# Kernel tuning notes

Measured on AMD Instinct MI355X. Metric: run time of the kernel, lower is better.

Reference implementation:

```python
import jax, jax.numpy as jnp
import numpy as np

EPS_BN = 1e-5
EPS_NORM = 1e-12

def _proj(x, W, g, b, m, v):
    # x: (B,C,N); W: (O,C) 1x1 conv; eval-mode BN per out channel; ReLU
    y = jnp.einsum('oc,bcn->bon', W, x)
    s = g / jnp.sqrt(v + EPS_BN)
    y = (y - m[None, :, None]) * s[None, :, None] + b[None, :, None]
    return jax.nn.relu(y)

def _l2norm(x, axis):
    n = jnp.sqrt(jnp.sum(x * x, axis=axis, keepdims=True))
    return x / jnp.maximum(n, EPS_NORM)

def setup_inputs() -> dict:
    key = jax.random.key(0)
    ks = jax.random.split(key, 8)
    B, C, H, W = 8, 256, 96, 96
    NS, K = 256, 64  # num_state, K
    X = jax.random.normal(ks[0], (B, C, H, W), dtype=jnp.float32)
    def mk(k, out_c):
        return (jax.random.normal(k, (out_c, C), dtype=jnp.float32) * 0.05,
                jnp.ones((out_c,), jnp.float32), jnp.zeros((out_c,), jnp.float32),
                jnp.zeros((out_c,), jnp.float32), jnp.ones((out_c,), jnp.float32))
    phi_w, phi_g, phi_b, phi_m, phi_v = mk(ks[1], K)
    theta_w, theta_g, theta_b, theta_m, theta_v = mk(ks[2], NS)
    rou_w, rou_g, rou_b, rou_m, rou_v = mk(ks[3], NS)
    val_w, val_g, val_b, val_m, val_v = mk(ks[4], NS)
    return dict(X=X,
                phi_w=phi_w, phi_g=phi_g, phi_b=phi_b, phi_m=phi_m, phi_v=phi_v,
                theta_w=theta_w, theta_g=theta_g, theta_b=theta_b, theta_m=theta_m, theta_v=theta_v,
                rou_w=rou_w, rou_g=rou_g, rou_b=rou_b, rou_m=rou_m, rou_v=rou_v,
                val_w=val_w, val_g=val_g, val_b=val_b, val_m=val_m, val_v=val_v)

def reference(X, phi_w, phi_g, phi_b, phi_m, phi_v,
              theta_w, theta_g, theta_b, theta_m, theta_v,
              rou_w, rou_g, rou_b, rou_m, rou_v,
              val_w, val_g, val_b, val_m, val_v):
    B, C, H, W = X.shape
    N = H * W
    x = X.reshape(B, C, N)
    x_phi = _proj(x, phi_w, phi_g, phi_b, phi_m, phi_v)          # (B,K,N)
    x_theta = _proj(x, theta_w, theta_g, theta_b, theta_m, theta_v)  # (B,S,N)
    x_theta = jax.nn.softmax(x_theta, axis=-1)                   # softmax over N
    discrib = jnp.einsum('bkn,bsn->bks', x_phi, x_theta)         # (B,K,S)
    x_rou = _proj(x, rou_w, rou_g, rou_b, rou_m, rou_v)          # (B,S,N)
    x_rou = jax.nn.softmax(x_rou, axis=1)                        # softmax over channels S
    Q = jnp.einsum('bks,bsn->bnk', discrib, x_rou)               # (B,N,K)
    Q = _l2norm(Q, axis=1)                                       # F.normalize dim=1 (over N)
    Q = jax.nn.softmax(Q, axis=-1)                               # softmax over K
    x_val = _proj(x, val_w, val_g, val_b, val_m, val_v)          # (B,S,N)
    # Z = sum_n Q[b,n,k]*x_val[b,s,n] / sum_n Q[b,n,k]  -- batched GEMM, no (B,S,N,K) blowup
    Znum = jnp.einsum('bsn,bnk->bsk', x_val, Q)                  # (B,S,K)
    Z = Znum / Q.sum(axis=1)[:, None, :]
    Z = _l2norm(Z, axis=1)                                       # F.normalize dim=1 (over S)
    return (Z, Q)
```

## Files before the change

### kernel.cpp

```cpp
#include <hip/hip_runtime.h>
#include <math.h>

#define B_ 8
#define C_ 256
#define N_ 9216
#define S_ 256
#define K_ 64
#define NCHUNK 36
#define TILE_KS (K_ * S_)
#define NC8 (N_ / 8)

typedef unsigned short ushort_t;
typedef __attribute__((ext_vector_type(8))) short bf16x8;
typedef __attribute__((ext_vector_type(4))) float f32x4;

static __device__ inline ushort_t f2bf(float x) {
    unsigned int u = __float_as_uint(x);
    unsigned int r = (u + 0x7fffu + ((u >> 16) & 1u)) >> 16;
    return (ushort_t)r;
}
static __device__ inline float bf2f(ushort_t u) {
    return __uint_as_float(((unsigned int)u) << 16);
}
static __device__ inline unsigned int cvtpk(float lo, float hi) {
    unsigned int r;
    asm("v_cvt_pk_bf16_f32 %0, %1, %2" : "=v"(r) : "v"(lo), "v"(hi));
    return r;
}

static __device__ inline uint4 expcell(uint4 u, float2 s) {
    uint4 r;
    unsigned int* up = (unsigned int*)&u;
    unsigned int* rp = (unsigned int*)&r;
#pragma unroll
    for (int q = 0; q < 4; ++q) {
        unsigned int x = up[q];
        float lo = __uint_as_float((x & 0xffffu) << 16);
        float hi = __uint_as_float(x & 0xffff0000u);
        rp[q] = cvtpk(__expf(lo - s.x) * s.y, __expf(hi - s.x) * s.y);
    }
    return r;
}

__global__ __launch_bounds__(256) void prep_w(
    const float* __restrict__ phi_w, const float* __restrict__ phi_g, const float* __restrict__ phi_b,
    const float* __restrict__ phi_m, const float* __restrict__ phi_v,
    const float* __restrict__ th_w, const float* __restrict__ th_g, const float* __restrict__ th_b,
    const float* __restrict__ th_m, const float* __restrict__ th_v,
    const float* __restrict__ ro_w, const float* __restrict__ ro_g, const float* __restrict__ ro_b,
    const float* __restrict__ ro_m, const float* __restrict__ ro_v,
    const float* __restrict__ va_w, const float* __restrict__ va_g, const float* __restrict__ va_b,
    const float* __restrict__ va_m, const float* __restrict__ va_v,
    ushort_t* __restrict__ Wt, float* __restrict__ be)
{
    const int o = blockIdx.x;
    const int t = threadIdx.x;
    const float *src, *g, *bb, *mm, *vv; int orel;
    if (o < 64)       { src = phi_w; g = phi_g; bb = phi_b; mm = phi_m; vv = phi_v; orel = o; }
    else if (o < 320) { src = th_w;  g = th_g;  bb = th_b;  mm = th_m;  vv = th_v;  orel = o - 64; }
    else if (o < 576) { src = ro_w;  g = ro_g;  bb = ro_b;  mm = ro_m;  vv = ro_v;  orel = o - 320; }
    else              { src = va_w;  g = va_g;  bb = va_b;  mm = va_m;  vv = va_v;  orel = o - 576; }
    const float s = g[orel] / sqrtf(vv[orel] + 1e-5f);
    const int ot = o >> 6, os = (o >> 4) & 3, st = t >> 5;
    const size_t flat = ((((size_t)ot * 8 + st) * 4 + os) * 64 + ((t >> 3) & 3) * 16 + (o & 15)) * 8 + (t & 7);
    Wt[flat] = f2bf(src[orel * C_ + t] * s);
    if (t == 0) be[o] = bb[orel] - mm[orel] * s;
}

__global__ __launch_bounds__(256) void xpose(
    const float* __restrict__ X, ushort_t* __restrict__ Xs)
{
    __shared__ float T[64][65];
    const int b = blockIdx.z, c0 = blockIdx.y * 64, n0 = blockIdx.x * 64;
    const int t = threadIdx.x;
#pragma unroll
    for (int p = 0; p < 4; ++p) {
        int c = p * 16 + (t >> 4), nn = (t & 15) * 4;
        float4 v = *(const float4*)&X[((size_t)b * C_ + c0 + c) * N_ + n0 + nn];
        T[c][nn] = v.x; T[c][nn + 1] = v.y; T[c][nn + 2] = v.z; T[c][nn + 3] = v.w;
    }
    __syncthreads();
#pragma unroll
    for (int p = 0; p < 4; ++p) {
        int nn = p * 16 + (t >> 4), cl = (t & 15) * 4;
        uint2 uu;
        uu.x = cvtpk(T[cl][nn], T[cl + 1][nn]);
        uu.y = cvtpk(T[cl + 2][nn], T[cl + 3][nn]);
        const int n = n0 + nn, c = c0 + cl;
        const int nt = n >> 8, nr = n & 255;
        const int st = c >> 5, g8 = (c >> 3) & 3, e = c & 7;
        const size_t base = ((((size_t)b * 36 + nt) * 8 + st) * 1024
                             + (nr >> 4) * 64 + g8 * 16 + (nr & 15)) * 8 + e;
        *(uint2*)&Xs[base] = uu;
    }
}

__global__ __launch_bounds__(256) void proj_mfma_all(
    const ushort_t* __restrict__ Wt, const float* __restrict__ be,
    const ushort_t* __restrict__ Xs,
    ushort_t* __restrict__ Pbf, ushort_t* __restrict__ Tbf,
    ushort_t* __restrict__ Vbf, ushort_t* __restrict__ Rt)
{
    __shared__ short sm[9216];
    const int t = threadIdx.x;
    const int l = t & 63, w = t >> 6;
    const int idx = blockIdx.x;
    const int xcd = idx & 7, pos = idx >> 3;
    const int vid = xcd * 468 + pos;
    const int ot  = vid % 13;
    const int r   = vid / 13;
    const int b   = r / 36;
    const int nt  = r % 36;
    const int n0  = nt * 256;
    const int o0  = ot * 64;

    const bf16x8* Wv = (const bf16x8*)Wt;
    const bf16x8* Xf = (const bf16x8*)Xs;
    const size_t xbase = ((size_t)b * 36 + nt) * 8192;
    const size_t wbase = (size_t)ot * 2048;
    const int boff = (l >> 4) * 16 + (l & 15);

    f32x4 zr = {0.f, 0.f, 0.f, 0.f};
    f32x4 acc[4][4];
#pragma unroll
    for (int i = 0; i < 4; ++i)
#pragma unroll
        for (int j = 0; j < 4; ++j) acc[i][j] = zr;

    bf16x8 A0[4], B0[4];
#pragma unroll
    for (int os = 0; os < 4; ++os) A0[os] = Wv[wbase + os * 64 + l];
#pragma unroll
    for (int j = 0; j < 4; ++j)   B0[j]  = Xf[xbase + (w * 4 + j) * 64 + boff];

#pragma unroll
    for (int st = 0; st < 8; ++st) {
        bf16x8 A1[4], B1[4];
        if (st < 7) {
#pragma unroll
            for (int os = 0; os < 4; ++os)
                A1[os] = Wv[wbase + (st + 1) * 256 + os * 64 + l];
#pragma unroll
            for (int j = 0; j < 4; ++j)
                B1[j] = Xf[xbase + (size_t)(st + 1) * 1024 + (w * 4 + j) * 64 + boff];
        }
#pragma unroll
        for (int os = 0; os < 4; ++os)
#pragma unroll
            for (int j = 0; j < 4; ++j)
                acc[os][j] = __builtin_amdgcn_mfma_f32_16x16x32_bf16(A0[os], B0[j], acc[os][j], 0, 0, 0);
#pragma unroll
        for (int os = 0; os < 4; ++os) A0[os] = A1[os];
#pragma unroll
        for (int j = 0; j < 4; ++j)   B0[j]  = B1[j];
    }

    if (o0 >= 320 && o0 < 576) {
        const int od = o0 - 320;
        ushort_t* Tt = (ushort_t*)sm + w * (32 * 72);
#pragma unroll
        for (int half = 0; half < 2; ++half) {
            __syncthreads();
#pragma unroll
            for (int jj = 0; jj < 2; ++jj) {
                const int j = half * 2 + jj;
                const int row = jj * 16 + (l & 15);
#pragma unroll
                for (int os = 0; os < 4; ++os) {
                    const int scol0 = os * 16 + (l >> 4) * 4;
                    const float b0 = be[o0 + scol0], b1 = be[o0 + scol0 + 1];
                    const float b2 = be[o0 + scol0 + 2], b3 = be[o0 + scol0 + 3];
                    unsigned int p0 = cvtpk(fmaxf(acc[os][j][0] + b0, 0.f),
                                            fmaxf(acc[os][j][1] + b1, 0.f));
                    unsigned int p1 = cvtpk(fmaxf(acc[os][j][2] + b2, 0.f),
                                            fmaxf(acc[os][j][3] + b3, 0.f));
                    *(unsigned int*)&Tt[row * 72 + scol0]     = p0;
                    *(unsigned int*)&Tt[row * 72 + scol0 + 2] = p1;
                }
            }
            __syncthreads();
#pragma unroll
            for (int p = 0; p < 4; ++p) {
                const int lrow = p * 8 + (l >> 3);
                uint4 v = *(const uint4*)&Tt[lrow * 72 + (l & 7) * 8];
                *(uint4*)&Rt[((size_t)b * N_ + n0 + w * 64 + half * 32 + lrow) * 256 + od + (l & 7) * 8] = v;
            }
        }
    } else {
        ushort_t* dst; int od, osz;
        if (o0 < 64)       { dst = Pbf; od = o0;       osz = 64;  }
        else if (o0 < 320) { dst = Tbf; od = o0 - 64;  osz = 256; }
        else               { dst = Vbf; od = o0 - 576; osz = 256; }
        ushort_t* Tw = (ushort_t*)sm + w * (32 * 68);
        const int c = l & 15;
#pragma unroll
        for (int half = 0; half < 2; ++half) {
            __syncthreads();
#pragma unroll
            for (int osl = 0; osl < 2; ++osl) {
                const int os = half * 2 + osl;
#pragma unroll
                for (int r2 = 0; r2 < 4; ++r2) {
                    const int lrow = osl * 16 + (l >> 4) * 4 + r2;
                    const int orow = half * 32 + lrow;
                    const float bias = be[o0 + orow];
                    unsigned int p0 = cvtpk(fmaxf(acc[os][0][r2] + bias, 0.f),
                                            fmaxf(acc[os][1][r2] + bias, 0.f));
                    unsigned int p1 = cvtpk(fmaxf(acc[os][2][r2] + bias, 0.f),
                                            fmaxf(acc[os][3][r2] + bias, 0.f));
                    Tw[lrow * 68 + c]      = (ushort_t)p0;
                    Tw[lrow * 68 + 16 + c] = (ushort_t)(p0 >> 16);
                    Tw[lrow * 68 + 32 + c] = (ushort_t)p1;
                    Tw[lrow * 68 + 48 + c] = (ushort_t)(p1 >> 16);
                }
            }
            __syncthreads();
#pragma unroll
            for (int i = 0; i < 8; ++i) {
                const int lrow = i * 4 + (l >> 4);
                ushort4 v = *(const ushort4*)&Tw[lrow * 68 + (l & 15) * 4];
                *(ushort4*)&dst[((size_t)(b * osz + od + half * 32 + lrow)) * N_ + n0 + w * 64 + (l & 15) * 4] = v;
            }
        }
    }
}

__global__ __launch_bounds__(256) void rowstat_n(
    const ushort_t* __restrict__ T, float* __restrict__ st2)
{
    const int row = blockIdx.x;
    const ushort4* p = (const ushort4*)(T + (size_t)row * N_);
    const int t = threadIdx.x;
    float v[36];
    float mx = -INFINITY;
#pragma unroll
    for (int i = 0; i < 9; ++i) {
        ushort4 u = p[t + i * 256];
        v[i * 4 + 0] = bf2f(u.x); v[i * 4 + 1] = bf2f(u.y);
        v[i * 4 + 2] = bf2f(u.z); v[i * 4 + 3] = bf2f(u.w);
        mx = fmaxf(mx, fmaxf(fmaxf(v[i * 4], v[i * 4 + 1]), fmaxf(v[i * 4 + 2], v[i * 4 + 3])));
    }
    __shared__ float red[256];
    red[t] = mx; __syncthreads();
    for (int s2 = 128; s2 > 0; s2 >>= 1) {
        if (t < s2) red[t] = fmaxf(red[t], red[t + s2]);
        __syncthreads();
    }
    mx = red[0]; __syncthreads();
    float sum = 0.f;
#pragma unroll
    for (int i = 0; i < 36; ++i) sum += __expf(v[i] - mx);
    red[t] = sum; __syncthreads();
    for (int s2 = 128; s2 > 0; s2 >>= 1) {
        if (t < s2) red[t] += red[t + s2];
        __syncthreads();
    }
    if (t == 0) ((float2*)st2)[row] = make_float2(mx, 1.0f / red[0]);
}

__global__ __launch_bounds__(256) void rowstat_rt(
    const ushort_t* __restrict__ R, float* __restrict__ st2r)
{
    const int w = threadIdx.x >> 6, l = threadIdx.x & 63;
    const size_t row0 = (size_t)blockIdx.x * 32 + w * 8;
    for (int r = 0; r < 8; ++r) {
        const ushort4* p = (const ushort4*)(R + (row0 + r) * 256);
        ushort4 u = p[l];
        float f0 = bf2f(u.x), f1 = bf2f(u.y), f2 = bf2f(u.z), f3 = bf2f(u.w);
        float mx = fmaxf(fmaxf(f0, f1), fmaxf(f2, f3));
#pragma unroll
        for (int m = 1; m < 64; m <<= 1) mx = fmaxf(mx, __shfl_xor(mx, m));
        float s = __expf(f0 - mx) + __expf(f1 - mx) + __expf(f2 - mx) + __expf(f3 - mx);
#pragma unroll
        for (int m = 1; m < 64; m <<= 1) s += __shfl_xor(s, m);
        if (l == 0) ((float2*)st2r)[row0 + r] = make_float2(mx, 1.0f / s);
    }
}

__global__ __launch_bounds__(256) void ks_mfma(
    const ushort_t* __restrict__ A, const ushort_t* __restrict__ Bm,
    const float* __restrict__ st2, float* __restrict__ P)
{
    __shared__ short sm[32768];
    const int t = threadIdx.x;
    const int l = t & 63, w = t >> 6;
    const int chunk = blockIdx.x, b = blockIdx.y;
    const int ccell = chunk * 32;

    const uint4* Av = (const uint4*)A;
    const uint4* Bv = (const uint4*)Bm;
    const float2* S2 = (const float2*)st2;
    uint4* smv = (uint4*)sm;
    const bool doexp = (st2 != nullptr);

    uint4 wreg[8], xreg[8];
    float2 sreg[8];
#pragma unroll
    for (int i = 0; i < 8; ++i) {
        int cell = i * 256 + t;
        int osub = cell >> 9, g = (cell >> 4) & 31, oi = cell & 15;
        wreg[i] = Av[(size_t)(b * 64 + osub * 16 + oi) * NC8 + ccell + g];
    }
#pragma unroll
    for (int i = 0; i < 8; ++i) {
        int cell = i * 256 + t;
        int s = cell >> 7, g8 = (cell >> 4) & 7, ni = cell & 15;
        int row = s * 16 + ni;
        xreg[i] = Bv[(size_t)(b * 256 + row) * NC8 + ccell + g8];
        if (doexp) sreg[i] = S2[b * 256 + row];
    }
#pragma unroll
    for (int i = 0; i < 8; ++i) smv[i * 256 + t] = wreg[i];
#pragma unroll
    for (int i = 0; i < 8; ++i) smv[2048 + i * 256 + t] = doexp ? expcell(xreg[i], sreg[i]) : xreg[i];
    __syncthreads();

    f32x4 zr = {0.f, 0.f, 0.f, 0.f};
    f32x4 acc[4][4];
#pragma unroll
    for (int i = 0; i < 4; ++i)
#pragma unroll
        for (int j = 0; j < 4; ++j) acc[i][j] = zr;

    const bf16x8* smW = (const bf16x8*)sm;
    const bf16x8* smX = (const bf16x8*)(sm + 16384);

    for (int st = 0; st < 4; ++st) {
        if (st < 3) {
#pragma unroll
            for (int i = 0; i < 8; ++i) {
                int cell = i * 256 + t;
                int s = cell >> 7, g8 = (cell >> 4) & 7, ni = cell & 15;
                int row = s * 16 + ni;
                xreg[i] = Bv[(size_t)(b * 256 + row) * NC8 + ccell + (st + 1) * 8 + g8];
            }
        }
#pragma unroll
        for (int kgl = 0; kgl < 2; ++kgl) {
            const int kg = st * 2 + kgl;
            bf16x8 Af[4], Bf[4];
#pragma unroll
            for (int os = 0; os < 4; ++os)
                Af[os] = smW[(os * 32 + kg * 4 + (l >> 4)) * 16 + (l & 15)];
#pragma unroll
            for (int j = 0; j < 4; ++j)
                Bf[j] = smX[((w * 4 + j) * 8 + kgl * 4 + (l >> 4)) * 16 + (l & 15)];
#pragma unroll
            for (int os = 0; os < 4; ++os)
#pragma unroll
                for (int j = 0; j < 4; ++j)
                    acc[os][j] = __builtin_amdgcn_mfma_f32_16x16x32_bf16(Af[os], Bf[j], acc[os][j], 0, 0, 0);
        }
        __syncthreads();
        if (st < 3) {
#pragma unroll
            for (int i = 0; i < 8; ++i) smv[2048 + i * 256 + t] = doexp ? expcell(xreg[i], sreg[i]) : xreg[i];
            __syncthreads();
        }
    }

    float* Pb = P + ((size_t)(chunk * B_ + b)) * TILE_KS;
#pragma unroll
    for (int os = 0; os < 4; ++os)
#pragma unroll
        for (int r = 0; r < 4; ++r) {
            const int k = os * 16 + (l >> 4) * 4 + r;
#pragma unroll
            for (int j = 0; j < 4; ++j)
                Pb[k * 256 + (w * 4 + j) * 16 + (l & 15)] = acc[os][j][r];
        }
}

__global__ __launch_bounds__(256) void qt_mfma(
    const ushort_t* __restrict__ Dbf,
    const ushort_t* __restrict__ Rraw,
    const float* __restrict__ st2r,
    float* __restrict__ Qraw,
    float* __restrict__ Nrm)
{
    __shared__ short sm[32768];
    const int t = threadIdx.x;
    const int l = t & 63, w = t >> 6;
    const int b = blockIdx.x / 36;
    const int n0 = (blockIdx.x % 36) * 256;

    const uint4* Av = (const uint4*)Dbf;
    const uint4* Xv = (const uint4*)Rraw;
    const float2* S2 = (const float2*)st2r;
    uint4* smv = (uint4*)sm;

    uint4 wreg[8], xreg[8];
    float2 sreg[8];
#pragma unroll
    for (int i = 0; i < 8; ++i) {
        int cell = i * 256 + t;
        int osub = cell >> 9, g = (cell >> 4) & 31, oi = cell & 15;
        wreg[i] = Av[(size_t)(b * 64 + osub * 16 + oi) * 32 + g];
    }
#pragma unroll
    for (int i = 0; i < 8; ++i) {
        int cell = i * 256 + t;
        int s = cell >> 7, g8 = (cell >> 4) & 7, ni = cell & 15;
        xreg[i] = Xv[((size_t)b * N_ + n0 + s * 16 + ni) * 32 + g8];
        sreg[i] = S2[(size_t)b * N_ + n0 + s * 16 + ni];
    }
#pragma unroll
    for (int i = 0; i < 8; ++i) smv[i * 256 + t] = wreg[i];
#pragma unroll
    for (int i = 0; i < 8; ++i) smv[2048 + i * 256 + t] = expcell(xreg[i], sreg[i]);
    __syncthreads();

    f32x4 zr = {0.f, 0.f, 0.f, 0.f};
    f32x4 acc[4][4];
#pragma unroll
    for (int i = 0; i < 4; ++i)
#pragma unroll
        for (int j = 0; j < 4; ++j) acc[i][j] = zr;

    const bf16x8* smW = (const bf16x8*)sm;
    const bf16x8* smX = (const bf16x8*)(sm + 16384);

    for (int st = 0; st < 4; ++st) {
        if (st < 3) {
#pragma unroll
            for (int i = 0; i < 8; ++i) {
                int cell = i * 256 + t;
                int s = cell >> 7, g8 = (cell >> 4) & 7, ni = cell & 15;
                xreg[i] = Xv[((size_t)b * N_ + n0 + s * 16 + ni) * 32 + (st + 1) * 8 + g8];
            }
        }
#pragma unroll
        for (int kgl = 0; kgl < 2; ++kgl) {
            const int kg = st * 2 + kgl;
            bf16x8 Af[4], Bf[4];
#pragma unroll
            for (int os = 0; os < 4; ++os)
                Af[os] = smW[(os * 32 + kg * 4 + (l >> 4)) * 16 + (l & 15)];
#pragma unroll
            for (int j = 0; j < 4; ++j)
                Bf[j] = smX[((w * 4 + j) * 8 + kgl * 4 + (l >> 4)) * 16 + (l & 15)];
#pragma unroll
            for (int os = 0; os < 4; ++os)
#pragma unroll
                for (int j = 0; j < 4; ++j)
                    acc[os][j] = __builtin_amdgcn_mfma_f32_16x16x32_bf16(Af[os], Bf[j], acc[os][j], 0, 0, 0);
        }
        __syncthreads();
        if (st < 3) {
#pragma unroll
            for (int i = 0; i < 8; ++i) smv[2048 + i * 256 + t] = expcell(xreg[i], sreg[i]);
            __syncthreads();
        }
    }

    float* snrm = (float*)sm + 9216;
    __syncthreads();
    if (t < 64) snrm[t] = 0.f;
    __syncthreads();
#pragma unroll
    for (int os = 0; os < 4; ++os)
#pragma unroll
        for (int r = 0; r < 4; ++r) {
            float p = 0.f;
#pragma unroll
            for (int j = 0; j < 4; ++j) p = fmaf(acc[os][j][r], acc[os][j][r], p);
#pragma unroll
            for (int m = 1; m < 16; m <<= 1) p += __shfl_xor(p, m);
            if ((l & 15) == 0) atomicAdd(&snrm[os * 16 + (l >> 4) * 4 + r], p);
        }
    float* Tw = (float*)sm + w * 2304;
#pragma unroll
    for (int h = 0; h < 2; ++h) {
        __syncthreads();
#pragma unroll
        for (int os = 0; os < 4; ++os)
#pragma unroll
            for (int r = 0; r < 4; ++r) {
                const int kcol = os * 16 + (l >> 4) * 4 + r;
#pragma unroll
                for (int jj = 0; jj < 2; ++jj)
                    Tw[(jj * 16 + (l & 15)) * 72 + kcol] = acc[os][h * 2 + jj][r];
            }
        __syncthreads();
#pragma unroll
        for (int i = 0; i < 8; ++i) {
            const int lrow = i * 4 + (l >> 4);
            f32x4 v = *(const f32x4*)&Tw[lrow * 72 + (l & 15) * 4];
            *(f32x4*)&Qraw[((size_t)b * N_ + n0 + w * 64 + h * 32 + lrow) * 64 + (l & 15) * 4] = v;
        }
    }
    __syncthreads();
    if (t < 64) atomicAdd(&Nrm[b * 64 + t], snrm[t]);
}

__global__ __launch_bounds__(256) void chunk_reduce_bf(
    const float* __restrict__ P, ushort_t* __restrict__ outb)
{
    const int i4 = blockIdx.x * 256 + threadIdx.x;
    float4 s = make_float4(0.f, 0.f, 0.f, 0.f);
#pragma unroll
    for (int c = 0; c < NCHUNK; ++c) {
        float4 v = ((const float4*)P)[(size_t)c * (B_ * TILE_KS / 4) + i4];
        s.x += v.x; s.y += v.y; s.z += v.z; s.w += v.w;
    }
    uint2 uu;
    uu.x = cvtpk(s.x, s.y);
    uu.y = cvtpk(s.z, s.w);
    ((uint2*)outb)[i4] = uu;
}
__global__ __launch_bounds__(256) void chunk_reduce_f(
    const float* __restrict__ P, float* __restrict__ outf)
{
    const int i4 = blockIdx.x * 256 + threadIdx.x;
    float4 s = make_float4(0.f, 0.f, 0.f, 0.f);
#pragma unroll
    for (int c = 0; c < NCHUNK; ++c) {
        float4 v = ((const float4*)P)[(size_t)c * (B_ * TILE_KS / 4) + i4];
        s.x += v.x; s.y += v.y; s.z += v.z; s.w += v.w;
    }
    ((float4*)outf)[i4] = s;
}

__global__ __launch_bounds__(256) void q_final(
    const float* __restrict__ Qraw, const float* __restrict__ Nrm,
    float* __restrict__ Qout, ushort_t* __restrict__ Qbf)
{
    __shared__ ushort_t Tq[64 * 256];
    __shared__ float invn[64];
    const int b = blockIdx.y;
    const int n0 = blockIdx.x * 256;
    const int t = threadIdx.x;
    const int l = t & 63, w = t >> 6;
    if (t < 64) invn[t] = 1.0f / fmaxf(sqrtf(Nrm[b * 64 + t]), 1e-12f);
    __syncthreads();
    const size_t base = ((size_t)b * N_ + n0 + t) * 64;
    float q[64];
#pragma unroll
    for (int kk = 0; kk < 16; ++kk) {
        f32x4 v = *(const f32x4*)&Qraw[base + kk * 4];
        q[kk * 4 + 0] = v[0]; q[kk * 4 + 1] = v[1]; q[kk * 4 + 2] = v[2]; q[kk * 4 + 3] = v[3];
    }
    float mx = -INFINITY;
#pragma unroll
    for (int k = 0; k < 64; ++k) { q[k] *= invn[k]; mx = fmaxf(mx, q[k]); }
    float sum = 0.f;
#pragma unroll
    for (int k = 0; k < 64; ++k) { q[k] = __expf(q[k] - mx); sum += q[k]; }
    const float inv = 1.0f / sum;
#pragma unroll
    for (int kk = 0; kk < 16; ++kk) {
        f32x4 v = {q[kk * 4] * inv, q[kk * 4 + 1] * inv, q[kk * 4 + 2] * inv, q[kk * 4 + 3] * inv};
        *(f32x4*)&Qout[base + kk * 4] = v;
        q[kk * 4] = v[0]; q[kk * 4 + 1] = v[1]; q[kk * 4 + 2] = v[2]; q[kk * 4 + 3] = v[3];
    }
#pragma unroll
    for (int k = 0; k < 64; ++k) Tq[k * 256 + t] = f2bf(q[k]);
    __syncthreads();
#pragma unroll
    for (int kk = 0; kk < 16; ++kk) {
        const int k = kk * 4 + w;
        ushort4 v = *(const ushort4*)&Tq[k * 256 + l * 4];
        *(ushort4*)&Qbf[((size_t)b * 64 + k) * N_ + n0 + l * 4] = v;
    }
}

__global__ __launch_bounds__(256) void z_final(
    const float* __restrict__ ZnT, float* __restrict__ Z)
{
    __shared__ float red[256];
    __shared__ float invn[64];
    const int b = blockIdx.x;
    const int t = threadIdx.x;
    const float* Zb = ZnT + (size_t)b * TILE_KS;
    {
        const int k = t >> 2, qq = t & 3;
        float ss = 0.f;
        for (int j = 0; j < 64; ++j) {
            float v = Zb[k * 256 + qq * 64 + j];
            ss = fmaf(v, v, ss);
        }
        red[t] = ss;
    }
    __syncthreads();
    if ((t & 3) == 0) {
        float tot = red[t] + red[t + 1] + red[t + 2] + red[t + 3];
        invn[t >> 2] = 1.0f / fmaxf(sqrtf(tot), 1e-12f);
    }
    __syncthreads();
    {
        const int k = t & 63, w = t >> 6;
        const float sc = invn[k];
        for (int j = 0; j < 64; ++j) {
            int s = w * 64 + j;
            Z[((size_t)b * 256 + s) * 64 + k] = Zb[k * 256 + s] * sc;
        }
    }
}

extern "C" void kernel_launch(void* const* d_in, const int* in_sizes, int n_in,
                              void* d_out, int out_size, void* d_ws, size_t ws_size,
                              hipStream_t stream)
{
    const float* X       = (const float*)d_in[0];
    const float* phi_w   = (const float*)d_in[1];
    const float* phi_g   = (const float*)d_in[2];
    const float* phi_b   = (const float*)d_in[3];
    const float* phi_m   = (const float*)d_in[4];
    const float* phi_v   = (const float*)d_in[5];
    const float* theta_w = (const float*)d_in[6];
    const float* theta_g = (const float*)d_in[7];
    const float* theta_b = (const float*)d_in[8];
    const float* theta_m = (const float*)d_in[9];
    const float* theta_v = (const float*)d_in[10];
    const float* rou_w   = (const float*)d_in[11];
    const float* rou_g   = (const float*)d_in[12];
    const float* rou_b   = (const float*)d_in[13];
    const float* rou_m   = (const float*)d_in[14];
    const float* rou_v   = (const float*)d_in[15];
    const float* val_w   = (const float*)d_in[16];
    const float* val_g   = (const float*)d_in[17];
    const float* val_b   = (const float*)d_in[18];
    const float* val_m   = (const float*)d_in[19];
    const float* val_v   = (const float*)d_in[20];

    float* ws = (float*)d_ws;
    size_t off = 0;
    ushort_t* Xs  = (ushort_t*)(ws + off); off += (size_t)B_ * N_ * C_ / 2;
    ushort_t* Wt  = (ushort_t*)(ws + off); off += 832 * C_ / 2;
    float* be     = ws + off; off += 832;
    float* st2    = ws + off; off += 2 * B_ * 256;
    float* st2r   = ws + off; off += 2 * B_ * N_;
    ushort_t* Pbf = (ushort_t*)(ws + off); off += (size_t)B_ * 64 * N_ / 2;
    ushort_t* Tbf = (ushort_t*)(ws + off); off += (size_t)B_ * 256 * N_ / 2;
    ushort_t* Vbf = (ushort_t*)(ws + off); off += (size_t)B_ * 256 * N_ / 2;
    ushort_t* Rt  = (ushort_t*)(ws + off); off += (size_t)B_ * N_ * 256 / 2;
    ushort_t* Qbf = (ushort_t*)(ws + off); off += (size_t)B_ * 64 * N_ / 2;
    ushort_t* Dbf = (ushort_t*)(ws + off); off += (size_t)B_ * 64 * 256 / 2;
    float* part   = ws + off; off += (size_t)NCHUNK * B_ * TILE_KS;
    float* Qraw   = ws + off; off += (size_t)B_ * N_ * 64;
    float* ZnT    = ws + off; off += (size_t)B_ * TILE_KS;
    float* Nrm    = ws + off; off += B_ * 64;

    float* Zout = (float*)d_out;
    float* Qout = Zout + (size_t)B_ * S_ * K_;

    hipMemsetAsync(Nrm, 0, B_ * 64 * sizeof(float), stream);

    prep_w<<<832, 256, 0, stream>>>(phi_w, phi_g, phi_b, phi_m, phi_v,
                                    theta_w, theta_g, theta_b, theta_m, theta_v,
                                    rou_w, rou_g, rou_b, rou_m, rou_v,
                                    val_w, val_g, val_b, val_m, val_v, Wt, be);
    xpose<<<dim3(N_ / 64, C_ / 64, B_), 256, 0, stream>>>(X, Xs);

    proj_mfma_all<<<3744, 256, 0, stream>>>(Wt, be, Xs, Pbf, Tbf, Vbf, Rt);

    rowstat_n<<<B_ * 256, 256, 0, stream>>>(Tbf, st2);
    rowstat_rt<<<B_ * N_ / 32, 256, 0, stream>>>(Rt, st2r);

    ks_mfma<<<dim3(NCHUNK, B_), 256, 0, stream>>>(Pbf, Tbf, st2, part);
    chunk_reduce_bf<<<B_ * TILE_KS / 1024, 256, 0, stream>>>(part, Dbf);

    qt_mfma<<<36 * B_, 256, 0, stream>>>(Dbf, Rt, st2r, Qraw, Nrm);
    q_final<<<dim3(36, B_), 256, 0, stream>>>(Qraw, Nrm, Qout, Qbf);

    ks_mfma<<<dim3(NCHUNK, B_), 256, 0, stream>>>(Qbf, Vbf, (const float*)nullptr, part);
    chunk_reduce_f<<<B_ * TILE_KS / 1024, 256, 0, stream>>>(part, ZnT);
    z_final<<<B_, 256, 0, stream>>>(ZnT, Zout);
}
```

Measured before the change: 201.4 us.

## Keep X tile resident in registers and loop over all output tiles per block

The projection kernel now assigns each block a 128-column slice of one batch and loads that X slice into registers once. It then iterates over all 13 output-channel tiles, streaming weights with a one-step prefetch. Epilogues use a double-buffered LDS region with wider 16-byte stores. This removes the 13-fold re-reading of X across blocks, but cuts the grid from 3744 to 576 blocks and drops the XCD-aware mapping, which risks lower occupancy, more register pressure and a serial weight-load chain.

```diff
diff --git a/kernel.cpp b/kernel.cpp
--- a/kernel.cpp
+++ b/kernel.cpp
@@ -101,125 +101,113 @@
     ushort_t* __restrict__ Pbf, ushort_t* __restrict__ Tbf,
     ushort_t* __restrict__ Vbf, ushort_t* __restrict__ Rt)
 {
-    __shared__ short sm[9216];
+    __shared__ short sm[18432];
     const int t = threadIdx.x;
     const int l = t & 63, w = t >> 6;
-    const int idx = blockIdx.x;
-    const int xcd = idx & 7, pos = idx >> 3;
-    const int vid = xcd * 468 + pos;
-    const int ot  = vid % 13;
-    const int r   = vid / 13;
-    const int b   = r / 36;
-    const int nt  = r % 36;
-    const int n0  = nt * 256;
-    const int o0  = ot * 64;
+    const int b   = blockIdx.x & 7;
+    const int nt2 = blockIdx.x >> 3;
+    const int nt  = nt2 >> 1, half = nt2 & 1;
+    const int n0  = nt2 * 128;
 
     const bf16x8* Wv = (const bf16x8*)Wt;
     const bf16x8* Xf = (const bf16x8*)Xs;
-    const size_t xbase = ((size_t)b * 36 + nt) * 8192;
-    const size_t wbase = (size_t)ot * 2048;
-    const int boff = (l >> 4) * 16 + (l & 15);
-
-    f32x4 zr = {0.f, 0.f, 0.f, 0.f};
-    f32x4 acc[4][4];
-#pragma unroll
-    for (int i = 0; i < 4; ++i)
-#pragma unroll
-        for (int j = 0; j < 4; ++j) acc[i][j] = zr;
-
-    bf16x8 A0[4], B0[4];
-#pragma unroll
-    for (int os = 0; os < 4; ++os) A0[os] = Wv[wbase + os * 64 + l];
-#pragma unroll
-    for (int j = 0; j < 4; ++j)   B0[j]  = Xf[xbase + (w * 4 + j) * 64 + boff];
-
-#pragma unroll
-    for (int st = 0; st < 8; ++st) {
-        bf16x8 A1[4], B1[4];
-        if (st < 7) {
+    const size_t xsbase = ((size_t)b * 36 + nt) * 8192;
+
+    bf16x8 Bx[8][2];
+#pragma unroll
+    for (int st = 0; st < 8; ++st)
+#pragma unroll
+        for (int nj = 0; nj < 2; ++nj)
+            Bx[st][nj] = Xf[xsbase + st * 1024 + (half * 8 + w * 2 + nj) * 64 + l];
+
+    bf16x8 A0[4], A1[4];
+#pragma unroll
+    for (int os = 0; os < 4; ++os) A0[os] = Wv[(size_t)os * 64 + l];
+
+    for (int ot = 0; ot < 13; ++ot) {
+        const int o0 = ot * 64;
+        f32x4 zr = {0.f, 0.f, 0.f, 0.f};
+        f32x4 acc[4][2];
+#pragma unroll
+        for (int os = 0; os < 4; ++os)
+#pragma unroll
+            for (int nj = 0; nj < 2; ++nj) acc[os][nj] = zr;
+
+#pragma unroll
+        for (int st = 0; st < 8; ++st) {
+            const int step = ot * 8 + st;
+            if (step < 103) {
+#pragma unroll
+                for (int os = 0; os < 4; ++os)
+                    A1[os] = Wv[(size_t)((step + 1) * 4 + os) * 64 + l];
+            }
 #pragma unroll
             for (int os = 0; os < 4; ++os)
-                A1[os] = Wv[wbase + (st + 1) * 256 + os * 64 + l];
-#pragma unroll
-            for (int j = 0; j < 4; ++j)
-                B1[j] = Xf[xbase + (size_t)(st + 1) * 1024 + (w * 4 + j) * 64 + boff];
-        }
-#pragma unroll
-        for (int os = 0; os < 4; ++os)
-#pragma unroll
-            for (int j = 0; j < 4; ++j)
-                acc[os][j] = __builtin_amdgcn_mfma_f32_16x16x32_bf16(A0[os], B0[j], acc[os][j], 0, 0, 0);
-#pragma unroll
-        for (int os = 0; os < 4; ++os) A0[os] = A1[os];
-#pragma unroll
-        for (int j = 0; j < 4; ++j)   B0[j]  = B1[j];
-    }
-
-    if (o0 >= 320 && o0 < 576) {
-        const int od = o0 - 320;
-        ushort_t* Tt = (ushort_t*)sm + w * (32 * 72);
-#pragma unroll
-        for (int half = 0; half < 2; ++half) {
+#pragma unroll
+                for (int nj = 0; nj < 2; ++nj)
+                    acc[os][nj] = __builtin_amdgcn_mfma_f32_16x16x32_bf16(A0[os], Bx[st][nj], acc[os][nj], 0, 0, 0);
+#pragma unroll
+            for (int os = 0; os < 4; ++os) A0[os] = A1[os];
+        }
+
+        ushort_t* Lb = (ushort_t*)sm + (ot & 1) * 9216;
+        if (ot >= 5 && ot < 9) {
+#pragma unroll
+            for (int os = 0; os < 4; ++os) {
+                const int sc0 = os * 16 + (l >> 4) * 4;
+                const float b0 = be[o0 + sc0],     b1 = be[o0 + sc0 + 1];
+                const float b2 = be[o0 + sc0 + 2], b3 = be[o0 + sc0 + 3];
+#pragma unroll
+                for (int nj = 0; nj < 2; ++nj) {
+                    const int nl = w * 32 + nj * 16 + (l & 15);
+                    unsigned int p0 = cvtpk(fmaxf(acc[os][nj][0] + b0, 0.f),
+                                            fmaxf(acc[os][nj][1] + b1, 0.f));
+                    unsigned int p1 = cvtpk(fmaxf(acc[os][nj][2] + b2, 0.f),
+                                            fmaxf(acc[os][nj][3] + b3, 0.f));
+                    *(unsigned int*)&Lb[nl * 72 + sc0]     = p0;
+                    *(unsigned int*)&Lb[nl * 72 + sc0 + 2] = p1;
+                }
+            }
             __syncthreads();
-#pragma unroll
-            for (int jj = 0; jj < 2; ++jj) {
-                const int j = half * 2 + jj;
-                const int row = jj * 16 + (l & 15);
-#pragma unroll
-                for (int os = 0; os < 4; ++os) {
-                    const int scol0 = os * 16 + (l >> 4) * 4;
-                    const float b0 = be[o0 + scol0], b1 = be[o0 + scol0 + 1];
-                    const float b2 = be[o0 + scol0 + 2], b3 = be[o0 + scol0 + 3];
-                    unsigned int p0 = cvtpk(fmaxf(acc[os][j][0] + b0, 0.f),
-                                            fmaxf(acc[os][j][1] + b1, 0.f));
-                    unsigned int p1 = cvtpk(fmaxf(acc[os][j][2] + b2, 0.f),
-                                            fmaxf(acc[os][j][3] + b3, 0.f));
-                    *(unsigned int*)&Tt[row * 72 + scol0]     = p0;
-                    *(unsigned int*)&Tt[row * 72 + scol0 + 2] = p1;
+            const int od = o0 - 320;
+#pragma unroll
+            for (int i = 0; i < 4; ++i) {
+                const int f = i * 256 + t;
+                const int row = f >> 3, seg = f & 7;
+                uint4 v = *(const uint4*)&Lb[row * 72 + seg * 8];
+                *(uint4*)&Rt[((size_t)b * N_ + n0 + row) * 256 + od + seg * 8] = v;
+            }
+        } else {
+            ushort_t* dst; int od, osz;
+            if (ot == 0)     { dst = Pbf; od = 0;        osz = 64;  }
+            else if (ot < 5) { dst = Tbf; od = o0 - 64;  osz = 256; }
+            else             { dst = Vbf; od = o0 - 576; osz = 256; }
+            const int c = l & 15;
+#pragma unroll
+            for (int os = 0; os < 4; ++os) {
+                const int or0 = os * 16 + (l >> 4) * 4;
+                const float b0 = be[o0 + or0],     b1 = be[o0 + or0 + 1];
+                const float b2 = be[o0 + or0 + 2], b3 = be[o0 + or0 + 3];
+#pragma unroll
+                for (int nj = 0; nj < 2; ++nj) {
+                    const int nl = w * 32 + nj * 16 + c;
+                    unsigned int p0 = cvtpk(fmaxf(acc[os][nj][0] + b0, 0.f),
+                                            fmaxf(acc[os][nj][1] + b1, 0.f));
+                    unsigned int p1 = cvtpk(fmaxf(acc[os][nj][2] + b2, 0.f),
+                                            fmaxf(acc[os][nj][3] + b3, 0.f));
+                    Lb[(or0    ) * 136 + nl] = (ushort_t)p0;
+                    Lb[(or0 + 1) * 136 + nl] = (ushort_t)(p0 >> 16);
+                    Lb[(or0 + 2) * 136 + nl] = (ushort_t)p1;
+                    Lb[(or0 + 3) * 136 + nl] = (ushort_t)(p1 >> 16);
                 }
             }
             __syncthreads();
 #pragma unroll
-            for (int p = 0; p < 4; ++p) {
-                const int lrow = p * 8 + (l >> 3);
-                uint4 v = *(const uint4*)&Tt[lrow * 72 + (l & 7) * 8];
-                *(uint4*)&Rt[((size_t)b * N_ + n0 + w * 64 + half * 32 + lrow) * 256 + od + (l & 7) * 8] = v;
-            }
-        }
-    } else {
-        ushort_t* dst; int od, osz;
-        if (o0 < 64)       { dst = Pbf; od = o0;       osz = 64;  }
-        else if (o0 < 320) { dst = Tbf; od = o0 - 64;  osz = 256; }
-        else               { dst = Vbf; od = o0 - 576; osz = 256; }
-        ushort_t* Tw = (ushort_t*)sm + w * (32 * 68);
-        const int c = l & 15;
-#pragma unroll
-        for (int half = 0; half < 2; ++half) {
-            __syncthreads();
-#pragma unroll
-            for (int osl = 0; osl < 2; ++osl) {
-                const int os = half * 2 + osl;
-#pragma unroll
-                for (int r2 = 0; r2 < 4; ++r2) {
-                    const int lrow = osl * 16 + (l >> 4) * 4 + r2;
-                    const int orow = half * 32 + lrow;
-                    const float bias = be[o0 + orow];
-                    unsigned int p0 = cvtpk(fmaxf(acc[os][0][r2] + bias, 0.f),
-                                            fmaxf(acc[os][1][r2] + bias, 0.f));
-                    unsigned int p1 = cvtpk(fmaxf(acc[os][2][r2] + bias, 0.f),
-                                            fmaxf(acc[os][3][r2] + bias, 0.f));
-                    Tw[lrow * 68 + c]      = (ushort_t)p0;
-                    Tw[lrow * 68 + 16 + c] = (ushort_t)(p0 >> 16);
-                    Tw[lrow * 68 + 32 + c] = (ushort_t)p1;
-                    Tw[lrow * 68 + 48 + c] = (ushort_t)(p1 >> 16);
-                }
-            }
-            __syncthreads();
-#pragma unroll
-            for (int i = 0; i < 8; ++i) {
-                const int lrow = i * 4 + (l >> 4);
-                ushort4 v = *(const ushort4*)&Tw[lrow * 68 + (l & 15) * 4];
-                *(ushort4*)&dst[((size_t)(b * osz + od + half * 32 + lrow)) * N_ + n0 + w * 64 + (l & 15) * 4] = v;
+            for (int i = 0; i < 4; ++i) {
+                const int f = i * 256 + t;
+                const int row = f >> 4, seg = f & 15;
+                uint4 v = *(const uint4*)&Lb[row * 136 + seg * 8];
+                *(uint4*)&dst[((size_t)(b * osz + od + row)) * N_ + n0 + seg * 8] = v;
             }
         }
     }
@@ -652,7 +640,7 @@
                                     val_w, val_g, val_b, val_m, val_v, Wt, be);
     xpose<<<dim3(N_ / 64, C_ / 64, B_), 256, 0, stream>>>(X, Xs);
 
-    proj_mfma_all<<<3744, 256, 0, stream>>>(Wt, be, Xs, Pbf, Tbf, Vbf, Rt);
+    proj_mfma_all<<<576, 256, 0, stream>>>(Wt, be, Xs, Pbf, Tbf, Vbf, Rt);
 
     rowstat_n<<<B_ * 256, 256, 0, stream>>>(Tbf, st2);
     rowstat_rt<<<B_ * N_ / 32, 256, 0, stream>>>(Rt, st2r);
```

After: 305.0 us. +51.5%, slower.

## Fuse channel-softmax row stats into qt_mfma and store intermediates in bf16

Applied to the files above, without the earlier changes.

Removes the separate rowstat_rt kernel by computing per-position max and inverse sum of the rou projection inside qt_mfma, keeping them in shared memory. The first ks_mfma now writes its per-chunk partials as bf16 for the bf16 reduce kernel, and the unnormalized Q is stored in bf16 instead of fp32, so q_final reads half the bytes. This cuts one launch and a large share of the intermediate global traffic. In exchange qt_mfma rereads the R rows and does extra reduction work, and partial sums and Q logits lose precision.

```diff
diff --git a/kernel.cpp b/kernel.cpp
--- a/kernel.cpp
+++ b/kernel.cpp
@@ -258,28 +258,9 @@
     if (t == 0) ((float2*)st2)[row] = make_float2(mx, 1.0f / red[0]);
 }
 
-__global__ __launch_bounds__(256) void rowstat_rt(
-    const ushort_t* __restrict__ R, float* __restrict__ st2r)
-{
-    const int w = threadIdx.x >> 6, l = threadIdx.x & 63;
-    const size_t row0 = (size_t)blockIdx.x * 32 + w * 8;
-    for (int r = 0; r < 8; ++r) {
-        const ushort4* p = (const ushort4*)(R + (row0 + r) * 256);
-        ushort4 u = p[l];
-        float f0 = bf2f(u.x), f1 = bf2f(u.y), f2 = bf2f(u.z), f3 = bf2f(u.w);
-        float mx = fmaxf(fmaxf(f0, f1), fmaxf(f2, f3));
-#pragma unroll
-        for (int m = 1; m < 64; m <<= 1) mx = fmaxf(mx, __shfl_xor(mx, m));
-        float s = __expf(f0 - mx) + __expf(f1 - mx) + __expf(f2 - mx) + __expf(f3 - mx);
-#pragma unroll
-        for (int m = 1; m < 64; m <<= 1) s += __shfl_xor(s, m);
-        if (l == 0) ((float2*)st2r)[row0 + r] = make_float2(mx, 1.0f / s);
-    }
-}
-
 __global__ __launch_bounds__(256) void ks_mfma(
     const ushort_t* __restrict__ A, const ushort_t* __restrict__ Bm,
-    const float* __restrict__ st2, float* __restrict__ P)
+    const float* __restrict__ st2, float* __restrict__ P, int obf16)
 {
     __shared__ short sm[32768];
     const int t = threadIdx.x;
@@ -359,26 +340,42 @@
         }
     }
 
-    float* Pb = P + ((size_t)(chunk * B_ + b)) * TILE_KS;
-#pragma unroll
-    for (int os = 0; os < 4; ++os)
-#pragma unroll
-        for (int r = 0; r < 4; ++r) {
-            const int k = os * 16 + (l >> 4) * 4 + r;
-#pragma unroll
-            for (int j = 0; j < 4; ++j)
-                Pb[k * 256 + (w * 4 + j) * 16 + (l & 15)] = acc[os][j][r];
-        }
+    if (obf16) {
+        ushort_t* Pb = (ushort_t*)P + ((size_t)(chunk * B_ + b)) * TILE_KS;
+#pragma unroll
+        for (int os = 0; os < 4; ++os)
+#pragma unroll
+            for (int r = 0; r < 4; ++r) {
+                const int k = os * 16 + (l >> 4) * 4 + r;
+                unsigned int p0 = cvtpk(acc[os][0][r], acc[os][1][r]);
+                unsigned int p1 = cvtpk(acc[os][2][r], acc[os][3][r]);
+                Pb[k * 256 + w * 64 + 0  + (l & 15)] = (ushort_t)p0;
+                Pb[k * 256 + w * 64 + 16 + (l & 15)] = (ushort_t)(p0 >> 16);
+                Pb[k * 256 + w * 64 + 32 + (l & 15)] = (ushort_t)p1;
+                Pb[k * 256 + w * 64 + 48 + (l & 15)] = (ushort_t)(p1 >> 16);
+            }
+    } else {
+        float* Pb = P + ((size_t)(chunk * B_ + b)) * TILE_KS;
+#pragma unroll
+        for (int os = 0; os < 4; ++os)
+#pragma unroll
+            for (int r = 0; r < 4; ++r) {
+                const int k = os * 16 + (l >> 4) * 4 + r;
+#pragma unroll
+                for (int j = 0; j < 4; ++j)
+                    Pb[k * 256 + (w * 4 + j) * 16 + (l & 15)] = acc[os][j][r];
+            }
+    }
 }
 
 __global__ __launch_bounds__(256) void qt_mfma(
     const ushort_t* __restrict__ Dbf,
     const ushort_t* __restrict__ Rraw,
-    const float* __restrict__ st2r,
-    float* __restrict__ Qraw,
+    ushort_t* __restrict__ Qraw,
     float* __restrict__ Nrm)
 {
-    __shared__ short sm[32768];
+    __shared__ short sm[33792];
+    float* stat = (float*)sm + 16384;
     const int t = threadIdx.x;
     const int l = t & 63, w = t >> 6;
     const int b = blockIdx.x / 36;
@@ -386,11 +383,9 @@
 
     const uint4* Av = (const uint4*)Dbf;
     const uint4* Xv = (const uint4*)Rraw;
-    const float2* S2 = (const float2*)st2r;
     uint4* smv = (uint4*)sm;
 
     uint4 wreg[8], xreg[8];
-    float2 sreg[8];
 #pragma unroll
     for (int i = 0; i < 8; ++i) {
         int cell = i * 256 + t;
@@ -402,12 +397,32 @@
         int cell = i * 256 + t;
         int s = cell >> 7, g8 = (cell >> 4) & 7, ni = cell & 15;
         xreg[i] = Xv[((size_t)b * N_ + n0 + s * 16 + ni) * 32 + g8];
-        sreg[i] = S2[(size_t)b * N_ + n0 + s * 16 + ni];
-    }
+    }
+
+    for (int r = 0; r < 64; ++r) {
+        const int nl = w * 64 + r;
+        const uint2* prow = (const uint2*)(Rraw + ((size_t)b * N_ + n0 + nl) * 256);
+        uint2 u = prow[l];
+        float f0 = bf2f((ushort_t)u.x), f1 = bf2f(u.x >> 16);
+        float f2 = bf2f((ushort_t)u.y), f3 = bf2f(u.y >> 16);
+        float mx = fmaxf(fmaxf(f0, f1), fmaxf(f2, f3));
+#pragma unroll
+        for (int m = 1; m < 64; m <<= 1) mx = fmaxf(mx, __shfl_xor(mx, m));
+        float s = __expf(f0 - mx) + __expf(f1 - mx) + __expf(f2 - mx) + __expf(f3 - mx);
+#pragma unroll
+        for (int m = 1; m < 64; m <<= 1) s += __shfl_xor(s, m);
+        if (l == 0) { stat[nl] = mx; stat[256 + nl] = 1.0f / s; }
+    }
+    __syncthreads();
+
 #pragma unroll
     for (int i = 0; i < 8; ++i) smv[i * 256 + t] = wreg[i];
 #pragma unroll
-    for (int i = 0; i < 8; ++i) smv[2048 + i * 256 + t] = expcell(xreg[i], sreg[i]);
+    for (int i = 0; i < 8; ++i) {
+        int cell = i * 256 + t;
+        int row = (cell >> 7) * 16 + (cell & 15);
+        smv[2048 + i * 256 + t] = expcell(xreg[i], make_float2(stat[row], stat[256 + row]));
+    }
     __syncthreads();
 
     f32x4 zr = {0.f, 0.f, 0.f, 0.f};
@@ -448,7 +463,11 @@
         __syncthreads();
         if (st < 3) {
 #pragma unroll
-            for (int i = 0; i < 8; ++i) smv[2048 + i * 256 + t] = expcell(xreg[i], sreg[i]);
+            for (int i = 0; i < 8; ++i) {
+                int cell = i * 256 + t;
+                int row = (cell >> 7) * 16 + (cell & 15);
+                smv[2048 + i * 256 + t] = expcell(xreg[i], make_float2(stat[row], stat[256 + row]));
+            }
             __syncthreads();
         }
     }
@@ -486,7 +505,10 @@
         for (int i = 0; i < 8; ++i) {
             const int lrow = i * 4 + (l >> 4);
             f32x4 v = *(const f32x4*)&Tw[lrow * 72 + (l & 15) * 4];
-            *(f32x4*)&Qraw[((size_t)b * N_ + n0 + w * 64 + h * 32 + lrow) * 64 + (l & 15) * 4] = v;
+            uint2 uu;
+            uu.x = cvtpk(v[0], v[1]);
+            uu.y = cvtpk(v[2], v[3]);
+            *(uint2*)&Qraw[((size_t)b * N_ + n0 + w * 64 + h * 32 + lrow) * 64 + (l & 15) * 4] = uu;
         }
     }
     __syncthreads();
@@ -494,7 +516,23 @@
 }
 
 __global__ __launch_bounds__(256) void chunk_reduce_bf(
-    const float* __restrict__ P, ushort_t* __restrict__ outb)
+    const ushort_t* __restrict__ P, ushort_t* __restrict__ outb)
+{
+    const int i2 = blockIdx.x * 256 + threadIdx.x;
+    float s0 = 0.f, s1 = 0.f, s2 = 0.f, s3 = 0.f;
+#pragma unroll
+    for (int c = 0; c < NCHUNK; ++c) {
+        uint2 u = ((const uint2*)P)[(size_t)c * (B_ * TILE_KS / 4) + i2];
+        s0 += bf2f((ushort_t)u.x); s1 += bf2f(u.x >> 16);
+        s2 += bf2f((ushort_t)u.y); s3 += bf2f(u.y >> 16);
+    }
+    uint2 o;
+    o.x = cvtpk(s0, s1);
+    o.y = cvtpk(s2, s3);
+    ((uint2*)outb)[i2] = o;
+}
+__global__ __launch_bounds__(256) void chunk_reduce_f(
+    const float* __restrict__ P, float* __restrict__ outf)
 {
     const int i4 = blockIdx.x * 256 + threadIdx.x;
     float4 s = make_float4(0.f, 0.f, 0.f, 0.f);
@@ -503,26 +541,11 @@
         float4 v = ((const float4*)P)[(size_t)c * (B_ * TILE_KS / 4) + i4];
         s.x += v.x; s.y += v.y; s.z += v.z; s.w += v.w;
     }
-    uint2 uu;
-    uu.x = cvtpk(s.x, s.y);
-    uu.y = cvtpk(s.z, s.w);
-    ((uint2*)outb)[i4] = uu;
-}
-__global__ __launch_bounds__(256) void chunk_reduce_f(
-    const float* __restrict__ P, float* __restrict__ outf)
-{
-    const int i4 = blockIdx.x * 256 + threadIdx.x;
-    float4 s = make_float4(0.f, 0.f, 0.f, 0.f);
-#pragma unroll
-    for (int c = 0; c < NCHUNK; ++c) {
-        float4 v = ((const float4*)P)[(size_t)c * (B_ * TILE_KS / 4) + i4];
-        s.x += v.x; s.y += v.y; s.z += v.z; s.w += v.w;
-    }
     ((float4*)outf)[i4] = s;
 }
 
 __global__ __launch_bounds__(256) void q_final(
-    const float* __restrict__ Qraw, const float* __restrict__ Nrm,
+    const ushort_t* __restrict__ Qraw, const float* __restrict__ Nrm,
     float* __restrict__ Qout, ushort_t* __restrict__ Qbf)
 {
     __shared__ ushort_t Tq[64 * 256];
@@ -533,12 +556,15 @@
     const int l = t & 63, w = t >> 6;
     if (t < 64) invn[t] = 1.0f / fmaxf(sqrtf(Nrm[b * 64 + t]), 1e-12f);
     __syncthreads();
-    const size_t base = ((size_t)b * N_ + n0 + t) * 64;
+    const uint4* q4 = (const uint4*)(Qraw + ((size_t)b * N_ + n0 + t) * 64);
     float q[64];
 #pragma unroll
-    for (int kk = 0; kk < 16; ++kk) {
-        f32x4 v = *(const f32x4*)&Qraw[base + kk * 4];
-        q[kk * 4 + 0] = v[0]; q[kk * 4 + 1] = v[1]; q[kk * 4 + 2] = v[2]; q[kk * 4 + 3] = v[3];
+    for (int kk = 0; kk < 8; ++kk) {
+        uint4 u = q4[kk];
+        q[kk * 8 + 0] = bf2f((ushort_t)u.x); q[kk * 8 + 1] = bf2f(u.x >> 16);
+        q[kk * 8 + 2] = bf2f((ushort_t)u.y); q[kk * 8 + 3] = bf2f(u.y >> 16);
+        q[kk * 8 + 4] = bf2f((ushort_t)u.z); q[kk * 8 + 5] = bf2f(u.z >> 16);
+        q[kk * 8 + 6] = bf2f((ushort_t)u.w); q[kk * 8 + 7] = bf2f(u.w >> 16);
     }
     float mx = -INFINITY;
 #pragma unroll
@@ -547,6 +573,7 @@
 #pragma unroll
     for (int k = 0; k < 64; ++k) { q[k] = __expf(q[k] - mx); sum += q[k]; }
     const float inv = 1.0f / sum;
+    const size_t base = ((size_t)b * N_ + n0 + t) * 64;
 #pragma unroll
     for (int kk = 0; kk < 16; ++kk) {
         f32x4 v = {q[kk * 4] * inv, q[kk * 4 + 1] * inv, q[kk * 4 + 2] * inv, q[kk * 4 + 3] * inv};
@@ -629,7 +656,6 @@
     ushort_t* Wt  = (ushort_t*)(ws + off); off += 832 * C_ / 2;
     float* be     = ws + off; off += 832;
     float* st2    = ws + off; off += 2 * B_ * 256;
-    float* st2r   = ws + off; off += 2 * B_ * N_;
     ushort_t* Pbf = (ushort_t*)(ws + off); off += (size_t)B_ * 64 * N_ / 2;
     ushort_t* Tbf = (ushort_t*)(ws + off); off += (size_t)B_ * 256 * N_ / 2;
     ushort_t* Vbf = (ushort_t*)(ws + off); off += (size_t)B_ * 256 * N_ / 2;
@@ -637,7 +663,7 @@
     ushort_t* Qbf = (ushort_t*)(ws + off); off += (size_t)B_ * 64 * N_ / 2;
     ushort_t* Dbf = (ushort_t*)(ws + off); off += (size_t)B_ * 64 * 256 / 2;
     float* part   = ws + off; off += (size_t)NCHUNK * B_ * TILE_KS;
-    float* Qraw   = ws + off; off += (size_t)B_ * N_ * 64;
+    ushort_t* Qraw = (ushort_t*)(ws + off); off += (size_t)B_ * N_ * 64 / 2;
     float* ZnT    = ws + off; off += (size_t)B_ * TILE_KS;
     float* Nrm    = ws + off; off += B_ * 64;
 
@@ -655,15 +681,14 @@
     proj_mfma_all<<<3744, 256, 0, stream>>>(Wt, be, Xs, Pbf, Tbf, Vbf, Rt);
 
     rowstat_n<<<B_ * 256, 256, 0, stream>>>(Tbf, st2);
-    rowstat_rt<<<B_ * N_ / 32, 256, 0, stream>>>(Rt, st2r);
-
-    ks_mfma<<<dim3(NCHUNK, B_), 256, 0, stream>>>(Pbf, Tbf, st2, part);
-    chunk_reduce_bf<<<B_ * TILE_KS / 1024, 256, 0, stream>>>(part, Dbf);
-
-    qt_mfma<<<36 * B_, 256, 0, stream>>>(Dbf, Rt, st2r, Qraw, Nrm);
+
+    ks_mfma<<<dim3(NCHUNK, B_), 256, 0, stream>>>(Pbf, Tbf, st2, part, 1);
+    chunk_reduce_bf<<<B_ * TILE_KS / 1024, 256, 0, stream>>>((const ushort_t*)part, Dbf);
+
+    qt_mfma<<<36 * B_, 256, 0, stream>>>(Dbf, Rt, Qraw, Nrm);
     q_final<<<dim3(36, B_), 256, 0, stream>>>(Qraw, Nrm, Qout, Qbf);
 
-    ks_mfma<<<dim3(NCHUNK, B_), 256, 0, stream>>>(Qbf, Vbf, (const float*)nullptr, part);
+    ks_mfma<<<dim3(NCHUNK, B_), 256, 0, stream>>>(Qbf, Vbf, (const float*)nullptr, part, 0);
     chunk_reduce_f<<<B_ * TILE_KS / 1024, 256, 0, stream>>>(part, ZnT);
     z_final<<<B_, 256, 0, stream>>>(ZnT, Zout);
 }
```

Result: slower. 232.8 us (+15.6%).
